# Kernel optimization log

Measured on AMD Instinct MI355X. Metric: run time of the kernel, lower is better.

The kernel has to match this reference:

```python
import jax, jax.numpy as jnp
import numpy as np

B, DIN, DM, N, L, H = 4, 256, 256, 256, 64, 4
LH = L // H  # d_k per head = 16


def setup_inputs() -> dict:
    key = jax.random.key(0)
    ks = jax.random.split(key, 11)
    randn = lambda k, s: jax.random.normal(k, s, dtype=jnp.float32)
    return {
        "X_Query": randn(ks[0], (B, DIN, N, L)),
        "X_Key": randn(ks[1], (B, DIN, N, L)),
        "X_Value": randn(ks[2], (B, DIN, N, L)),
        "Wq": randn(ks[3], (DM, DIN)) * 0.05,
        "bq": randn(ks[4], (DM,)) * 0.05,
        "Wk": randn(ks[5], (DM, DIN)) * 0.05,
        "bk": randn(ks[6], (DM,)) * 0.05,
        "Wv": randn(ks[7], (DM, DIN)) * 0.05,
        "bv": randn(ks[8], (DM,)) * 0.05,
        "Wo": randn(ks[9], (DM, DM)) * 0.05,
        "bo": randn(ks[10], (DM,)) * 0.05,
    }


def _conv1x1(x, W, b):
    # x: (B, Cin, N, L); 1x1 Conv2d == per-position linear over channels
    return jnp.einsum("bcnl,oc->bonl", x, W) + b[None, :, None, None]


def reference(X_Query, X_Key, X_Value, Wq, bq, Wk, bk, Wv, bv, Wo, bo):
    q = _conv1x1(X_Query, Wq, bq)  # (B, DM, N, L)
    k = _conv1x1(X_Key, Wk, bk)
    v = _conv1x1(X_Value, Wv, bv)
    # torch: chunk(num_heads, dim=-1) then cat(dim=0) -> head axis from L split
    split = lambda x: x.reshape(B, DM, N, H, LH)
    qh, kh, vh = split(q), split(k), split(v)
    # attention over the CHANNEL axis (d_model x d_model scores per point/head)
    scale = 1.0 / np.sqrt(LH).astype(np.float32)
    scores = jnp.einsum("bdnhl,benhl->bnhde", qh, kh) * scale  # (B,N,H,DM,DM)
    p = jax.nn.softmax(scores, axis=-1)
    o = jnp.einsum("bnhde,benhl->bdnhl", p, vh)  # (B,DM,N,H,LH)
    attention_heads = o.reshape(B, DM, N, L)  # cat heads back along L
    return _conv1x1(attention_heads, Wo, bo)
```

## Files before the change

### kernel.cpp

```cpp
#include <hip/hip_runtime.h>


typedef unsigned int u32;
typedef unsigned short u16;
typedef __attribute__((ext_vector_type(8))) short s8v;
typedef __attribute__((ext_vector_type(16))) float f16v;

#define XB 0
#define QB 16384
#define KB 32768
#define VB 49152

__device__ __forceinline__ u16 f2bf(float x) {
  union { float f; u32 u; } c; c.f = x;
  return (u16)((c.u + 0x7FFFu + ((c.u >> 16) & 1u)) >> 16);
}
__device__ __forceinline__ u32 pk2(float a, float b) {
  return (u32)f2bf(a) | ((u32)f2bf(b) << 16);
}

__global__ void cvt_weights(const float* __restrict__ wq, const float* __restrict__ wk,
                            const float* __restrict__ wv, const float* __restrict__ wo,
                            u16* __restrict__ out) {
  int i = blockIdx.x * 256 + threadIdx.x;
  out[i]          = f2bf(wq[i]);
  out[i + 65536]  = f2bf(wk[i]);
  out[i + 131072] = f2bf(wv[i]);
  out[i + 196608] = f2bf(wo[i]);
}

__device__ __forceinline__ void stage_lin(const float* __restrict__ src, u16* lds,
                                          int dst, int tid) {
#pragma unroll
  for (int p = 0; p < 8; ++p) {
    int f4 = p * 512 + tid;
    int c = f4 >> 4;
    int l4 = (f4 & 15) << 2;
    const float4 v = *reinterpret_cast<const float4*>(src + c * 16384 + l4);
    uint2 w; w.x = pk2(v.x, v.y); w.y = pk2(v.z, v.w);
    *reinterpret_cast<uint2*>(&lds[dst + c * 64 + l4]) = w;
  }
}

__device__ __forceinline__ void lin_to_xb(u16* lds, int srcoff, int tid) {
  int l = tid & 63, cg = tid >> 6;
#pragma unroll
  for (int it = 0; it < 4; ++it) {
    int cb = (it << 3) + cg;
    int sb = srcoff + cb * 512 + l;
    u32 u0 = (u32)lds[sb]       | ((u32)lds[sb + 64]  << 16);
    u32 u1 = (u32)lds[sb + 128] | ((u32)lds[sb + 192] << 16);
    u32 u2 = (u32)lds[sb + 256] | ((u32)lds[sb + 320] << 16);
    u32 u3 = (u32)lds[sb + 384] | ((u32)lds[sb + 448] << 16);
    union { u32 u[4]; s8v v; } pw;
    pw.u[0] = u0; pw.u[1] = u1; pw.u[2] = u2; pw.u[3] = u3;
    *reinterpret_cast<s8v*>(&lds[XB + cb * 512 + l * 8]) = pw.v;
  }
}

__device__ __forceinline__ void proj_T(u16* lds, const u16* __restrict__ w,
                                       const float* __restrict__ bias, int dstoff,
                                       int wid, int lo, int hi) {
  const int o = wid * 32 + lo;
  f16v a0, a1;
#pragma unroll
  for (int i = 0; i < 16; ++i) { a0[i] = 0.f; a1[i] = 0.f; }
#pragma unroll
  for (int s = 0; s < 16; ++s) {
    const s8v bw = *reinterpret_cast<const s8v*>(w + o * 256 + s * 16 + hi * 8);
    const s8v x0 = *reinterpret_cast<const s8v*>(&lds[XB + (2 * s + hi) * 512 + lo * 8]);
    const s8v x1 = *reinterpret_cast<const s8v*>(&lds[XB + (2 * s + hi) * 512 + (32 + lo) * 8]);
    a0 = __builtin_amdgcn_mfma_f32_32x32x16_bf16(x0, bw, a0, 0, 0, 0);
    a1 = __builtin_amdgcn_mfma_f32_32x32x16_bf16(x1, bw, a1, 0, 0, 0);
  }
  const float bb = bias[o];
#pragma unroll
  for (int mt = 0; mt < 2; ++mt) {
    const f16v& ac = mt ? a1 : a0;
#pragma unroll
    for (int g = 0; g < 4; ++g) {
      uint2 wv2;
      wv2.x = pk2(ac[4 * g + 0] + bb, ac[4 * g + 1] + bb);
      wv2.y = pk2(ac[4 * g + 2] + bb, ac[4 * g + 3] + bb);
      *reinterpret_cast<uint2*>(&lds[dstoff + (4 * mt + g) * 2048 + o * 8 + hi * 4]) = wv2;
    }
  }
}

__device__ __forceinline__ void proj_V(u16* lds, const u16* __restrict__ w,
                                       const float* __restrict__ bias,
                                       int wid, int lo, int hi) {
  const int e0 = wid * 32;
  const int e = e0 + lo;
  f16v a0, a1;
#pragma unroll
  for (int i = 0; i < 16; ++i) { a0[i] = 0.f; a1[i] = 0.f; }
#pragma unroll
  for (int s = 0; s < 16; ++s) {
    const s8v aw = *reinterpret_cast<const s8v*>(w + e * 256 + s * 16 + hi * 8);
    const s8v x0 = *reinterpret_cast<const s8v*>(&lds[XB + (2 * s + hi) * 512 + lo * 8]);
    const s8v x1 = *reinterpret_cast<const s8v*>(&lds[XB + (2 * s + hi) * 512 + (32 + lo) * 8]);
    a0 = __builtin_amdgcn_mfma_f32_32x32x16_bf16(aw, x0, a0, 0, 0, 0);
    a1 = __builtin_amdgcn_mfma_f32_32x32x16_bf16(aw, x1, a1, 0, 0, 0);
  }
#pragma unroll
  for (int nt = 0; nt < 2; ++nt) {
    const f16v& ac = nt ? a1 : a0;
    const int l = nt * 32 + lo;
#pragma unroll
    for (int g = 0; g < 4; ++g) {
      const int eb = e0 + 8 * g + 4 * hi;
      uint2 wv2;
      wv2.x = pk2(ac[4 * g + 0] + bias[eb + 0], ac[4 * g + 1] + bias[eb + 1]);
      wv2.y = pk2(ac[4 * g + 2] + bias[eb + 2], ac[4 * g + 3] + bias[eb + 3]);
      *reinterpret_cast<uint2*>(&lds[VB + (4 * wid + g) * 512 + l * 8 + hi * 4]) = wv2;
    }
  }
}

__device__ __forceinline__ void proj_O(u16* lds, const u16* __restrict__ w,
                                       const float* __restrict__ bias,
                                       float* __restrict__ out, int obase,
                                       int wid, int lo, int hi) {
  const int o0 = wid * 32;
  const int o = o0 + lo;
  f16v a0, a1;
#pragma unroll
  for (int i = 0; i < 16; ++i) { a0[i] = 0.f; a1[i] = 0.f; }
#pragma unroll
  for (int s = 0; s < 16; ++s) {
    const s8v aw = *reinterpret_cast<const s8v*>(w + o * 256 + s * 16 + hi * 8);
    const s8v b0 = *reinterpret_cast<const s8v*>(&lds[XB + (2 * s + hi) * 512 + lo * 8]);
    const s8v b1 = *reinterpret_cast<const s8v*>(&lds[XB + (2 * s + hi) * 512 + (32 + lo) * 8]);
    a0 = __builtin_amdgcn_mfma_f32_32x32x16_bf16(aw, b0, a0, 0, 0, 0);
    a1 = __builtin_amdgcn_mfma_f32_32x32x16_bf16(aw, b1, a1, 0, 0, 0);
  }
#pragma unroll
  for (int nt = 0; nt < 2; ++nt) {
    const f16v& ac = nt ? a1 : a0;
    const int l = nt * 32 + lo;
#pragma unroll
    for (int r = 0; r < 16; ++r) {
      const int orow = o0 + (r & 3) + 8 * (r >> 2) + 4 * hi;
      out[obase + orow * 16384 + l] = ac[r] + bias[orow];
    }
  }
}

__global__ __launch_bounds__(512)
void mha_kernel(const float* __restrict__ xq, const float* __restrict__ xk,
                const float* __restrict__ xv, const u16* __restrict__ wb,
                const float* __restrict__ bq, const float* __restrict__ bk,
                const float* __restrict__ bv, const float* __restrict__ bo,
                float* __restrict__ out) {
  __shared__ __align__(16) u16 lds[65536];
  const int tid = threadIdx.x;
  const int lane = tid & 63;
  const int wid = tid >> 6;
  const int lo = lane & 31;
  const int hi = lane >> 5;
  const int b = blockIdx.x >> 8, n = blockIdx.x & 255;
  const int base = b * 4194304 + n * 64;

  stage_lin(xq + base, lds, QB, tid);
  __syncthreads();
  lin_to_xb(lds, QB, tid);
  __syncthreads();
  stage_lin(xk + base, lds, KB, tid);
  proj_T(lds, wb + 0, bq, QB, wid, lo, hi);
  __syncthreads();
  lin_to_xb(lds, KB, tid);
  __syncthreads();
  stage_lin(xv + base, lds, VB, tid);
  proj_T(lds, wb + 65536, bk, KB, wid, lo, hi);
  __syncthreads();
  lin_to_xb(lds, VB, tid);
  __syncthreads();
  proj_V(lds, wb + 131072, bv, wid, lo, hi);
  __syncthreads();

  f16v z16;
#pragma unroll
  for (int i = 0; i < 16; ++i) z16[i] = 0.f;

  for (int h = 0; h < 4; ++h) {
    const s8v qf = *reinterpret_cast<const s8v*>(&lds[QB + (2 * h + hi) * 2048 + (wid * 32 + lo) * 8]);
    f16v st[8];
#pragma unroll
    for (int et = 0; et < 8; ++et) {
      const s8v kf = *reinterpret_cast<const s8v*>(&lds[KB + (2 * h + hi) * 2048 + (et * 32 + lo) * 8]);
      st[et] = __builtin_amdgcn_mfma_f32_32x32x16_bf16(kf, qf, z16, 0, 0, 0);
    }
    float m = -3.0e38f;
#pragma unroll
    for (int et = 0; et < 8; ++et)
#pragma unroll
      for (int r = 0; r < 16; ++r) m = fmaxf(m, st[et][r]);
    m = fmaxf(m, __shfl_xor(m, 32));
    const float m4 = 0.25f * m;
    float sum = 0.f;
#pragma unroll
    for (int et = 0; et < 8; ++et)
#pragma unroll
      for (int r = 0; r < 16; ++r) {
        const float p = __expf(0.25f * st[et][r] - m4);
        st[et][r] = p;
        sum += p;
      }
    sum += __shfl_xor(sum, 32);
    const float rinv = 1.0f / sum;

    f16v ot;
#pragma unroll
    for (int i = 0; i < 16; ++i) ot[i] = 0.f;
#pragma unroll
    for (int s = 0; s < 16; ++s) {
      const int et = s >> 1, s8o = (s & 1) * 8;
      const s8v vf = *reinterpret_cast<const s8v*>(
          &lds[VB + (2 * s + hi) * 512 + (h * 16 + (lane & 15)) * 8]);
      const u32 x0 = pk2(st[et][s8o + 0], st[et][s8o + 1]);
      const u32 x1 = pk2(st[et][s8o + 2], st[et][s8o + 3]);
      const u32 y0 = pk2(st[et][s8o + 4], st[et][s8o + 5]);
      const u32 y1 = pk2(st[et][s8o + 6], st[et][s8o + 7]);
      const u32 sx0 = (u32)__shfl_xor((int)x0, 32);
      const u32 sx1 = (u32)__shfl_xor((int)x1, 32);
      const u32 sy0 = (u32)__shfl_xor((int)y0, 32);
      const u32 sy1 = (u32)__shfl_xor((int)y1, 32);
      union { u32 u[4]; s8v v; } bu;
      bu.u[0] = hi ? sy0 : x0;
      bu.u[1] = hi ? sy1 : x1;
      bu.u[2] = hi ? y0 : sx0;
      bu.u[3] = hi ? y1 : sx1;
      ot = __builtin_amdgcn_mfma_f32_32x32x16_bf16(vf, bu.v, ot, 0, 0, 0);
    }
#pragma unroll
    for (int r = 0; r < 8; ++r) {
      const int lh = (r & 3) + 8 * (r >> 2) + 4 * hi;
      const int l = h * 16 + lh;
      const int d = wid * 32 + lo;
      lds[XB + (d >> 3) * 512 + l * 8 + (d & 7)] = f2bf(ot[r] * rinv);
    }
  }
  __syncthreads();

  proj_O(lds, wb + 196608, bo, out, base, wid, lo, hi);
}

extern "C" void kernel_launch(void* const* d_in, const int* in_sizes, int n_in,
                              void* d_out, int out_size, void* d_ws, size_t ws_size,
                              hipStream_t stream) {
  const float* xq = (const float*)d_in[0];
  const float* xk = (const float*)d_in[1];
  const float* xv = (const float*)d_in[2];
  const float* wq = (const float*)d_in[3];
  const float* bq = (const float*)d_in[4];
  const float* wk = (const float*)d_in[5];
  const float* bk = (const float*)d_in[6];
  const float* wv = (const float*)d_in[7];
  const float* bv = (const float*)d_in[8];
  const float* wo = (const float*)d_in[9];
  const float* bo = (const float*)d_in[10];
  u16* wsb = (u16*)d_ws;
  float* out = (float*)d_out;

  cvt_weights<<<dim3(256), dim3(256), 0, stream>>>(wq, wk, wv, wo, wsb);
  mha_kernel<<<dim3(1024), dim3(512), 0, stream>>>(xq, xk, xv, wsb, bq, bk, bv, bo, out);
}
```

Measured before the change: 187.6 us.

## Split each point into two half-L blocks and use online softmax

Each block now handles 32 of the 64 L positions (two heads) instead of all 64, so the grid doubles and the LDS footprint drops from 128KB to about 66KB. The idea is to allow more blocks per CU. The staging buffer now uses a padded stride of 36 to reduce bank conflicts during the transpose. The attention loop switches to an online softmax that computes scores per 32-wide tile and rescales the accumulator, instead of holding all eight score tiles in registers, which should lower register pressure. In exchange, every weight matrix is re-read by twice as many blocks, and the rescaling adds exp and multiply work.

```diff
diff --git a/kernel.cpp b/kernel.cpp
--- a/kernel.cpp
+++ b/kernel.cpp
@@ -6,10 +6,12 @@
 typedef __attribute__((ext_vector_type(8))) short s8v;
 typedef __attribute__((ext_vector_type(16))) float f16v;
 
-#define XB 0
-#define QB 16384
-#define KB 32768
-#define VB 49152
+#define XS 0
+#define QT 8192
+#define KT 16384
+#define VT 24576
+#define LDS_TOT 33792
+#define LSTR 36
 
 __device__ __forceinline__ u16 f2bf(float x) {
   union { float f; u32 u; } c; c.f = x;
@@ -30,60 +32,54 @@
 }
 
 __device__ __forceinline__ void stage_lin(const float* __restrict__ src, u16* lds,
-                                          int dst, int tid) {
-#pragma unroll
-  for (int p = 0; p < 8; ++p) {
-    int f4 = p * 512 + tid;
-    int c = f4 >> 4;
-    int l4 = (f4 & 15) << 2;
+                                          int linoff, int tid) {
+#pragma unroll
+  for (int it = 0; it < 4; ++it) {
+    int f4 = it * 512 + tid;
+    int c = f4 >> 3;
+    int l4 = (f4 & 7) << 2;
     const float4 v = *reinterpret_cast<const float4*>(src + c * 16384 + l4);
     uint2 w; w.x = pk2(v.x, v.y); w.y = pk2(v.z, v.w);
-    *reinterpret_cast<uint2*>(&lds[dst + c * 64 + l4]) = w;
-  }
-}
-
-__device__ __forceinline__ void lin_to_xb(u16* lds, int srcoff, int tid) {
-  int l = tid & 63, cg = tid >> 6;
-#pragma unroll
-  for (int it = 0; it < 4; ++it) {
-    int cb = (it << 3) + cg;
-    int sb = srcoff + cb * 512 + l;
-    u32 u0 = (u32)lds[sb]       | ((u32)lds[sb + 64]  << 16);
-    u32 u1 = (u32)lds[sb + 128] | ((u32)lds[sb + 192] << 16);
-    u32 u2 = (u32)lds[sb + 256] | ((u32)lds[sb + 320] << 16);
-    u32 u3 = (u32)lds[sb + 384] | ((u32)lds[sb + 448] << 16);
+    *reinterpret_cast<uint2*>(&lds[linoff + c * LSTR + l4]) = w;
+  }
+}
+
+__device__ __forceinline__ void lin_to_xs(u16* lds, int linoff, int tid) {
+#pragma unroll
+  for (int it = 0; it < 2; ++it) {
+    int idx = it * 512 + tid;
+    int l = idx & 31, cb = idx >> 5;
+    int sb = linoff + cb * (8 * LSTR) + l;
+    u32 u0 = (u32)lds[sb]            | ((u32)lds[sb + LSTR]     << 16);
+    u32 u1 = (u32)lds[sb + 2 * LSTR] | ((u32)lds[sb + 3 * LSTR] << 16);
+    u32 u2 = (u32)lds[sb + 4 * LSTR] | ((u32)lds[sb + 5 * LSTR] << 16);
+    u32 u3 = (u32)lds[sb + 6 * LSTR] | ((u32)lds[sb + 7 * LSTR] << 16);
     union { u32 u[4]; s8v v; } pw;
     pw.u[0] = u0; pw.u[1] = u1; pw.u[2] = u2; pw.u[3] = u3;
-    *reinterpret_cast<s8v*>(&lds[XB + cb * 512 + l * 8]) = pw.v;
+    *reinterpret_cast<s8v*>(&lds[XS + cb * 256 + l * 8]) = pw.v;
   }
 }
 
 __device__ __forceinline__ void proj_T(u16* lds, const u16* __restrict__ w,
-                                       const float* __restrict__ bias, int dstoff,
+                                       const float* __restrict__ bias, int dst,
                                        int wid, int lo, int hi) {
   const int o = wid * 32 + lo;
-  f16v a0, a1;
-#pragma unroll
-  for (int i = 0; i < 16; ++i) { a0[i] = 0.f; a1[i] = 0.f; }
+  f16v a;
+#pragma unroll
+  for (int i = 0; i < 16; ++i) a[i] = 0.f;
 #pragma unroll
   for (int s = 0; s < 16; ++s) {
     const s8v bw = *reinterpret_cast<const s8v*>(w + o * 256 + s * 16 + hi * 8);
-    const s8v x0 = *reinterpret_cast<const s8v*>(&lds[XB + (2 * s + hi) * 512 + lo * 8]);
-    const s8v x1 = *reinterpret_cast<const s8v*>(&lds[XB + (2 * s + hi) * 512 + (32 + lo) * 8]);
-    a0 = __builtin_amdgcn_mfma_f32_32x32x16_bf16(x0, bw, a0, 0, 0, 0);
-    a1 = __builtin_amdgcn_mfma_f32_32x32x16_bf16(x1, bw, a1, 0, 0, 0);
+    const s8v xf = *reinterpret_cast<const s8v*>(&lds[XS + (2 * s + hi) * 256 + lo * 8]);
+    a = __builtin_amdgcn_mfma_f32_32x32x16_bf16(xf, bw, a, 0, 0, 0);
   }
   const float bb = bias[o];
 #pragma unroll
-  for (int mt = 0; mt < 2; ++mt) {
-    const f16v& ac = mt ? a1 : a0;
-#pragma unroll
-    for (int g = 0; g < 4; ++g) {
-      uint2 wv2;
-      wv2.x = pk2(ac[4 * g + 0] + bb, ac[4 * g + 1] + bb);
-      wv2.y = pk2(ac[4 * g + 2] + bb, ac[4 * g + 3] + bb);
-      *reinterpret_cast<uint2*>(&lds[dstoff + (4 * mt + g) * 2048 + o * 8 + hi * 4]) = wv2;
-    }
+  for (int g = 0; g < 4; ++g) {
+    uint2 wv2;
+    wv2.x = pk2(a[4 * g + 0] + bb, a[4 * g + 1] + bb);
+    wv2.y = pk2(a[4 * g + 2] + bb, a[4 * g + 3] + bb);
+    *reinterpret_cast<uint2*>(&lds[dst + g * 2048 + o * 8 + hi * 4]) = wv2;
   }
 }
 
@@ -92,58 +88,44 @@
                                        int wid, int lo, int hi) {
   const int e0 = wid * 32;
   const int e = e0 + lo;
-  f16v a0, a1;
-#pragma unroll
-  for (int i = 0; i < 16; ++i) { a0[i] = 0.f; a1[i] = 0.f; }
+  f16v a;
+#pragma unroll
+  for (int i = 0; i < 16; ++i) a[i] = 0.f;
 #pragma unroll
   for (int s = 0; s < 16; ++s) {
     const s8v aw = *reinterpret_cast<const s8v*>(w + e * 256 + s * 16 + hi * 8);
-    const s8v x0 = *reinterpret_cast<const s8v*>(&lds[XB + (2 * s + hi) * 512 + lo * 8]);
-    const s8v x1 = *reinterpret_cast<const s8v*>(&lds[XB + (2 * s + hi) * 512 + (32 + lo) * 8]);
-    a0 = __builtin_amdgcn_mfma_f32_32x32x16_bf16(aw, x0, a0, 0, 0, 0);
-    a1 = __builtin_amdgcn_mfma_f32_32x32x16_bf16(aw, x1, a1, 0, 0, 0);
-  }
-#pragma unroll
-  for (int nt = 0; nt < 2; ++nt) {
-    const f16v& ac = nt ? a1 : a0;
-    const int l = nt * 32 + lo;
-#pragma unroll
-    for (int g = 0; g < 4; ++g) {
-      const int eb = e0 + 8 * g + 4 * hi;
-      uint2 wv2;
-      wv2.x = pk2(ac[4 * g + 0] + bias[eb + 0], ac[4 * g + 1] + bias[eb + 1]);
-      wv2.y = pk2(ac[4 * g + 2] + bias[eb + 2], ac[4 * g + 3] + bias[eb + 3]);
-      *reinterpret_cast<uint2*>(&lds[VB + (4 * wid + g) * 512 + l * 8 + hi * 4]) = wv2;
-    }
+    const s8v xf = *reinterpret_cast<const s8v*>(&lds[XS + (2 * s + hi) * 256 + lo * 8]);
+    a = __builtin_amdgcn_mfma_f32_32x32x16_bf16(aw, xf, a, 0, 0, 0);
+  }
+#pragma unroll
+  for (int g = 0; g < 4; ++g) {
+    const int eb = e0 + 8 * g + 4 * hi;
+    uint2 wv2;
+    wv2.x = pk2(a[4 * g + 0] + bias[eb + 0], a[4 * g + 1] + bias[eb + 1]);
+    wv2.y = pk2(a[4 * g + 2] + bias[eb + 2], a[4 * g + 3] + bias[eb + 3]);
+    *reinterpret_cast<uint2*>(&lds[VT + (4 * wid + g) * 256 + lo * 8 + hi * 4]) = wv2;
   }
 }
 
 __device__ __forceinline__ void proj_O(u16* lds, const u16* __restrict__ w,
                                        const float* __restrict__ bias,
-                                       float* __restrict__ out, int obase,
+                                       float* __restrict__ out, long obase,
                                        int wid, int lo, int hi) {
   const int o0 = wid * 32;
   const int o = o0 + lo;
-  f16v a0, a1;
-#pragma unroll
-  for (int i = 0; i < 16; ++i) { a0[i] = 0.f; a1[i] = 0.f; }
+  f16v a;
+#pragma unroll
+  for (int i = 0; i < 16; ++i) a[i] = 0.f;
 #pragma unroll
   for (int s = 0; s < 16; ++s) {
     const s8v aw = *reinterpret_cast<const s8v*>(w + o * 256 + s * 16 + hi * 8);
-    const s8v b0 = *reinterpret_cast<const s8v*>(&lds[XB + (2 * s + hi) * 512 + lo * 8]);
-    const s8v b1 = *reinterpret_cast<const s8v*>(&lds[XB + (2 * s + hi) * 512 + (32 + lo) * 8]);
-    a0 = __builtin_amdgcn_mfma_f32_32x32x16_bf16(aw, b0, a0, 0, 0, 0);
-    a1 = __builtin_amdgcn_mfma_f32_32x32x16_bf16(aw, b1, a1, 0, 0, 0);
-  }
-#pragma unroll
-  for (int nt = 0; nt < 2; ++nt) {
-    const f16v& ac = nt ? a1 : a0;
-    const int l = nt * 32 + lo;
-#pragma unroll
-    for (int r = 0; r < 16; ++r) {
-      const int orow = o0 + (r & 3) + 8 * (r >> 2) + 4 * hi;
-      out[obase + orow * 16384 + l] = ac[r] + bias[orow];
-    }
+    const s8v bf = *reinterpret_cast<const s8v*>(&lds[XS + (2 * s + hi) * 256 + lo * 8]);
+    a = __builtin_amdgcn_mfma_f32_32x32x16_bf16(aw, bf, a, 0, 0, 0);
+  }
+#pragma unroll
+  for (int r = 0; r < 16; ++r) {
+    const int orow = o0 + (r & 3) + 8 * (r >> 2) + 4 * hi;
+    out[obase + orow * 16384 + lo] = a[r] + bias[orow];
   }
 }
 
@@ -153,28 +135,30 @@
                 const float* __restrict__ bq, const float* __restrict__ bk,
                 const float* __restrict__ bv, const float* __restrict__ bo,
                 float* __restrict__ out) {
-  __shared__ __align__(16) u16 lds[65536];
+  __shared__ __align__(16) u16 lds[LDS_TOT];
   const int tid = threadIdx.x;
   const int lane = tid & 63;
   const int wid = tid >> 6;
   const int lo = lane & 31;
   const int hi = lane >> 5;
-  const int b = blockIdx.x >> 8, n = blockIdx.x & 255;
-  const int base = b * 4194304 + n * 64;
-
-  stage_lin(xq + base, lds, QB, tid);
-  __syncthreads();
-  lin_to_xb(lds, QB, tid);
-  __syncthreads();
-  stage_lin(xk + base, lds, KB, tid);
-  proj_T(lds, wb + 0, bq, QB, wid, lo, hi);
-  __syncthreads();
-  lin_to_xb(lds, KB, tid);
-  __syncthreads();
-  stage_lin(xv + base, lds, VB, tid);
-  proj_T(lds, wb + 65536, bk, KB, wid, lo, hi);
-  __syncthreads();
-  lin_to_xb(lds, VB, tid);
+  const int hp = blockIdx.x & 1;
+  const int n = (blockIdx.x >> 1) & 255;
+  const int b = blockIdx.x >> 9;
+  const long base = (long)b * 4194304 + n * 64 + hp * 32;
+
+  stage_lin(xq + base, lds, KT, tid);
+  __syncthreads();
+  lin_to_xs(lds, KT, tid);
+  __syncthreads();
+  stage_lin(xk + base, lds, KT, tid);
+  proj_T(lds, wb + 0, bq, QT, wid, lo, hi);
+  __syncthreads();
+  lin_to_xs(lds, KT, tid);
+  __syncthreads();
+  stage_lin(xv + base, lds, VT, tid);
+  proj_T(lds, wb + 65536, bk, KT, wid, lo, hi);
+  __syncthreads();
+  lin_to_xs(lds, VT, tid);
   __syncthreads();
   proj_V(lds, wb + 131072, bv, wid, lo, hi);
   __syncthreads();
@@ -182,63 +166,72 @@
   f16v z16;
 #pragma unroll
   for (int i = 0; i < 16; ++i) z16[i] = 0.f;
-
-  for (int h = 0; h < 4; ++h) {
-    const s8v qf = *reinterpret_cast<const s8v*>(&lds[QB + (2 * h + hi) * 2048 + (wid * 32 + lo) * 8]);
-    f16v st[8];
+  const int l15 = lane & 15;
+
+#pragma unroll
+  for (int h = 0; h < 2; ++h) {
+    const s8v qf = *reinterpret_cast<const s8v*>(
+        &lds[QT + (2 * h + hi) * 2048 + (wid * 32 + lo) * 8]);
+    float m = -3.0e38f, sum = 0.f;
+    f16v ot;
+#pragma unroll
+    for (int i = 0; i < 16; ++i) ot[i] = 0.f;
+
 #pragma unroll
     for (int et = 0; et < 8; ++et) {
-      const s8v kf = *reinterpret_cast<const s8v*>(&lds[KB + (2 * h + hi) * 2048 + (et * 32 + lo) * 8]);
-      st[et] = __builtin_amdgcn_mfma_f32_32x32x16_bf16(kf, qf, z16, 0, 0, 0);
+      const s8v kf = *reinterpret_cast<const s8v*>(
+          &lds[KT + (2 * h + hi) * 2048 + (et * 32 + lo) * 8]);
+      f16v st = __builtin_amdgcn_mfma_f32_32x32x16_bf16(kf, qf, z16, 0, 0, 0);
+
+      float tmax = st[0];
+#pragma unroll
+      for (int i = 1; i < 16; ++i) tmax = fmaxf(tmax, st[i]);
+      tmax = fmaxf(tmax, __shfl_xor(tmax, 32));
+      const float mn = fmaxf(m, tmax);
+      const float f = __expf(0.25f * (m - mn));
+      m = mn;
+      sum *= f;
+#pragma unroll
+      for (int i = 0; i < 16; ++i) ot[i] *= f;
+      float ts = 0.f;
+#pragma unroll
+      for (int i = 0; i < 16; ++i) {
+        const float p = __expf(0.25f * (st[i] - m));
+        st[i] = p;
+        ts += p;
+      }
+      sum += ts;
+
+#pragma unroll
+      for (int s2 = 0; s2 < 2; ++s2) {
+        const int s = 2 * et + s2;
+        const s8v vf = *reinterpret_cast<const s8v*>(
+            &lds[VT + (2 * s + hi) * 256 + (h * 16 + l15) * 8]);
+        const int q = s2 * 8;
+        const u32 x0 = pk2(st[q + 0], st[q + 1]);
+        const u32 x1 = pk2(st[q + 2], st[q + 3]);
+        const u32 y0 = pk2(st[q + 4], st[q + 5]);
+        const u32 y1 = pk2(st[q + 6], st[q + 7]);
+        const u32 sx0 = (u32)__shfl_xor((int)x0, 32);
+        const u32 sx1 = (u32)__shfl_xor((int)x1, 32);
+        const u32 sy0 = (u32)__shfl_xor((int)y0, 32);
+        const u32 sy1 = (u32)__shfl_xor((int)y1, 32);
+        union { u32 u[4]; s8v v; } bu;
+        bu.u[0] = hi ? sy0 : x0;
+        bu.u[1] = hi ? sy1 : x1;
+        bu.u[2] = hi ? y0 : sx0;
+        bu.u[3] = hi ? y1 : sx1;
+        ot = __builtin_amdgcn_mfma_f32_32x32x16_bf16(vf, bu.v, ot, 0, 0, 0);
+      }
     }
-    float m = -3.0e38f;
-#pragma unroll
-    for (int et = 0; et < 8; ++et)
-#pragma unroll
-      for (int r = 0; r < 16; ++r) m = fmaxf(m, st[et][r]);
-    m = fmaxf(m, __shfl_xor(m, 32));
-    const float m4 = 0.25f * m;
-    float sum = 0.f;
-#pragma unroll
-    for (int et = 0; et < 8; ++et)
-#pragma unroll
-      for (int r = 0; r < 16; ++r) {
-        const float p = __expf(0.25f * st[et][r] - m4);
-        st[et][r] = p;
-        sum += p;
-      }
     sum += __shfl_xor(sum, 32);
     const float rinv = 1.0f / sum;
-
-    f16v ot;
-#pragma unroll
-    for (int i = 0; i < 16; ++i) ot[i] = 0.f;
-#pragma unroll
-    for (int s = 0; s < 16; ++s) {
-      const int et = s >> 1, s8o = (s & 1) * 8;
-      const s8v vf = *reinterpret_cast<const s8v*>(
-          &lds[VB + (2 * s + hi) * 512 + (h * 16 + (lane & 15)) * 8]);
-      const u32 x0 = pk2(st[et][s8o + 0], st[et][s8o + 1]);
-      const u32 x1 = pk2(st[et][s8o + 2], st[et][s8o + 3]);
-      const u32 y0 = pk2(st[et][s8o + 4], st[et][s8o + 5]);
-      const u32 y1 = pk2(st[et][s8o + 6], st[et][s8o + 7]);
-      const u32 sx0 = (u32)__shfl_xor((int)x0, 32);
-      const u32 sx1 = (u32)__shfl_xor((int)x1, 32);
-      const u32 sy0 = (u32)__shfl_xor((int)y0, 32);
-      const u32 sy1 = (u32)__shfl_xor((int)y1, 32);
-      union { u32 u[4]; s8v v; } bu;
-      bu.u[0] = hi ? sy0 : x0;
-      bu.u[1] = hi ? sy1 : x1;
-      bu.u[2] = hi ? y0 : sx0;
-      bu.u[3] = hi ? y1 : sx1;
-      ot = __builtin_amdgcn_mfma_f32_32x32x16_bf16(vf, bu.v, ot, 0, 0, 0);
-    }
 #pragma unroll
     for (int r = 0; r < 8; ++r) {
       const int lh = (r & 3) + 8 * (r >> 2) + 4 * hi;
       const int l = h * 16 + lh;
       const int d = wid * 32 + lo;
-      lds[XB + (d >> 3) * 512 + l * 8 + (d & 7)] = f2bf(ot[r] * rinv);
+      lds[XS + (d >> 3) * 256 + l * 8 + (d & 7)] = f2bf(ot[r] * rinv);
     }
   }
   __syncthreads();
@@ -264,5 +257,5 @@
   float* out = (float*)d_out;
 
   cvt_weights<<<dim3(256), dim3(256), 0, stream>>>(wq, wk, wv, wo, wsb);
-  mha_kernel<<<dim3(1024), dim3(512), 0, stream>>>(xq, xk, xv, wsb, bq, bk, bv, bo, out);
-}
+  mha_kernel<<<dim3(2048), dim3(512), 0, stream>>>(xq, xk, xv, wsb, bq, bk, bv, bo, out);
+}
```

After: 213.0 us. 13.6% more time.
